# Performance work log

Hardware: AMD Instinct MI355X
Metric: run time of the kernel (lower is better)

## Reference

```python
import jax, jax.numpy as jnp
import numpy as np

EPS = 1e-6
NEG = -1e9
W = 8          # chunk_size
H_MA = 4       # monotonic heads
H_CA = 1       # chunkwise heads
ADIM = 1024
SHARP = 1.0    # sharpening_factor
SCALE = float(np.sqrt(ADIM))


def moving_sum(x, back, forward):
    # windowed sum over last axis, window = back+forward+1 (small, fixed)
    K = x.shape[-1]
    pad = [(0, 0)] * (x.ndim - 1) + [(back, forward)]
    xp = jnp.pad(x, pad)
    out = xp[..., 0:K]
    for d in range(1, back + forward + 1):
        out = out + xp[..., d:d + K]
    return out


def exclusive_cumsum(x):
    z = jnp.zeros(x.shape[:-1] + (1,), x.dtype)
    return jnp.cumsum(jnp.concatenate([z, x[..., :-1]], axis=-1), axis=-1)


def setup_inputs():
    key0 = jax.random.key(0)
    ks = jax.random.split(key0, 12)
    B, K, Q, D = 16, 2000, 256, 1024
    nrm = lambda k, shp, s=1.0: jax.random.normal(k, shp, jnp.float32) * s
    aw_prev = jnp.zeros((B, H_MA, 1, K), jnp.float32).at[..., 0].set(1.0)
    return {
        'key': nrm(ks[0], (B, K, D)),
        'value': nrm(ks[1], (B, K, D)),
        'query': nrm(ks[2], (B, Q, D)),
        'mask': jnp.ones((B, Q, K), jnp.int32),
        'aw_prev': aw_prev,
        'Wk_ma': nrm(ks[3], (D, ADIM), 0.02), 'bk_ma': jnp.zeros((ADIM,), jnp.float32),
        'Wq_ma': nrm(ks[4], (D, ADIM), 0.02), 'bq_ma': jnp.zeros((ADIM,), jnp.float32),
        'r': jnp.full((1,), -4.0, jnp.float32),
        'Wk_ca': nrm(ks[5], (D, ADIM), 0.02), 'bk_ca': jnp.zeros((ADIM,), jnp.float32),
        'Wq_ca': nrm(ks[6], (D, ADIM), 0.02), 'bq_ca': jnp.zeros((ADIM,), jnp.float32),
        'Wv': nrm(ks[7], (D, ADIM), 0.02), 'bv': jnp.zeros((ADIM,), jnp.float32),
        'Wo': nrm(ks[8], (ADIM, D), 0.02), 'bo': jnp.zeros((D,), jnp.float32),
    }


def reference(key, value, query, mask, aw_prev,
              Wk_ma, bk_ma, Wq_ma, bq_ma, r,
              Wk_ca, bk_ca, Wq_ca, bq_ca, Wv, bv, Wo, bo):
    B, K, D = key.shape
    Q = query.shape[1]
    dk_ma = ADIM // H_MA
    H_tot = H_MA * H_CA
    dk_ca = ADIM // H_tot
    m = (mask[:, None] != 0)  # [B,1,Q,K]

    # ---- monotonic energy: [B,H_ma,Q,K]
    k_ma = (key @ Wk_ma + bk_ma).reshape(B, K, H_MA, dk_ma)
    q_ma = (query @ Wq_ma + bq_ma).reshape(B, Q, H_MA, dk_ma)
    e_ma = jnp.einsum('bqhd,bkhd->bhqk', q_ma, k_ma) / SCALE + r[0]
    e_ma = jnp.where(m, e_ma, NEG)

    # ---- monotonic alignment alpha (parallel training mode)
    p = jax.nn.sigmoid(e_ma)                                  # [B,H,Q,K]
    log1mp = jnp.log(jnp.clip(1.0 - p, EPS, 1.0))
    cp = jnp.exp(exclusive_cumsum(log1mp))                    # safe_cumprod(1-p)

    def step(aw, pc):
        p_i, cp_i = pc                                        # [B,H,K]
        denom = jnp.clip(cp_i, EPS, 1.0)
        aw_new = p_i * cp_i * jnp.cumsum(aw / denom, axis=-1)
        return aw_new, aw_new

    xs = (p.transpose(2, 0, 1, 3), cp.transpose(2, 0, 1, 3))  # [Q,B,H,K]
    _, alphas = jax.lax.scan(step, aw_prev[:, :, 0], xs)
    alpha = alphas.transpose(1, 2, 0, 3)                      # [B,H_ma,Q,K]

    # ---- chunk energy: [B,H_ma*H_ca,Q,K]
    k_ca = (key @ Wk_ca + bk_ca).reshape(B, K, H_tot, dk_ca)
    q_ca = (query @ Wq_ca + bq_ca).reshape(B, Q, H_tot, dk_ca)
    e_ca = jnp.einsum('bqhd,bkhd->bhqk', q_ca, k_ca) / SCALE
    e_ca = jnp.where(m, e_ca, NEG)

    # ---- soft chunkwise attention (moving-sum windowed softmax)
    u = e_ca.reshape(B, H_MA, H_CA, Q, K)
    a5 = alpha[:, :, None] * SHARP                            # [B,H_ma,1,Q,K]
    u = u - jnp.max(u, axis=-1, keepdims=True)
    se = jnp.clip(jnp.exp(u), 1e-5, None)
    denom = moving_sum(se, W - 1, 0)
    beta = se * moving_sum(a5 / denom, 0, W - 1)
    beta = beta.reshape(B, H_tot, Q, K)

    # ---- context + output projection
    v = (value @ Wv + bv).reshape(B, K, H_tot, dk_ca)
    cv = jnp.einsum('bhqk,bkhd->bqhd', beta, v).reshape(B, Q, ADIM)
    return cv @ Wo + bo
```

## Files before the change

### kernel.cpp

```cpp
#include <hip/hip_runtime.h>


typedef __bf16 bf16x8_t __attribute__((ext_vector_type(8)));
typedef float f32x4_t __attribute__((ext_vector_type(4)));
typedef unsigned short ushort8_t __attribute__((ext_vector_type(8)));
typedef unsigned short ushort4_t __attribute__((ext_vector_type(4)));
typedef unsigned int uint4_t __attribute__((ext_vector_type(4)));

__device__ __forceinline__ unsigned short f2bf(float x) {
  unsigned int u = __builtin_bit_cast(unsigned int, x);
  u += 0x7fffu + ((u >> 16) & 1u);
  return (unsigned short)(u >> 16);
}
__device__ __forceinline__ float bf2f(unsigned short h) {
  unsigned int u = ((unsigned int)h) << 16;
  return __builtin_bit_cast(float, u);
}

__device__ __forceinline__ void gld16(const unsigned short* g, unsigned short* l) {
  __builtin_amdgcn_global_load_lds(
      (const __attribute__((address_space(1))) void*)g,
      (__attribute__((address_space(3))) void*)l, 16, 0, 0);
}

__device__ __forceinline__ float wave_incl_scan(float x) {
  float v = x;
  int mv;
#define DPP_ADD(ctrl, rmask, bctrl)                                           \
  mv = __builtin_amdgcn_update_dpp(0, __builtin_bit_cast(int, v), ctrl,       \
                                   rmask, 0xf, bctrl);                        \
  v += __builtin_bit_cast(float, mv);
  DPP_ADD(0x111, 0xf, true);
  DPP_ADD(0x112, 0xf, true);
  DPP_ADD(0x114, 0xf, true);
  DPP_ADD(0x118, 0xf, true);
  DPP_ADD(0x142, 0xa, false);
  DPP_ADD(0x143, 0xc, false);
#undef DPP_ADD
  return v;
}

__device__ __forceinline__ float wave_max_bcast(float x) {
  const float NI = -__builtin_inff();
  float v = x;
  int mv;
#define DPP_MAX(ctrl, rmask)                                                  \
  mv = __builtin_amdgcn_update_dpp(__builtin_bit_cast(int, NI),               \
                                   __builtin_bit_cast(int, v), ctrl, rmask,   \
                                   0xf, false);                               \
  v = fmaxf(v, __builtin_bit_cast(float, mv));
  DPP_MAX(0x111, 0xf) DPP_MAX(0x112, 0xf) DPP_MAX(0x114, 0xf)
  DPP_MAX(0x118, 0xf) DPP_MAX(0x142, 0xa) DPP_MAX(0x143, 0xc)
#undef DPP_MAX
  int r = __builtin_amdgcn_readlane(__builtin_bit_cast(int, v), 63);
  return __builtin_bit_cast(float, r);
}

#define WSHR1(dst, src)                                                       \
  {                                                                           \
    int _t = __builtin_amdgcn_update_dpp(0, __builtin_bit_cast(int, src),     \
                                         0x138, 0xf, 0xf, true);              \
    dst = __builtin_bit_cast(float, _t);                                      \
  }
#define WSHL1(dst, src)                                                       \
  {                                                                           \
    int _t = __builtin_amdgcn_update_dpp(0, __builtin_bit_cast(int, src),     \
                                         0x130, 0xf, 0xf, true);              \
    dst = __builtin_bit_cast(float, _t);                                      \
  }

__device__ __forceinline__ void gemm_bt_tile(
    const unsigned short* __restrict__ A, long lda,
    const unsigned short* __restrict__ B, long ldb,
    int Kd, unsigned short* lA, unsigned short* lB, f32x4_t acc[4][4]) {
  const int tid = threadIdx.x;
  const int lane = tid & 63;
  const int wid = tid >> 6;
  const int wm = wid >> 1, wn = wid & 1;
  const int lr = lane & 15, quad = lane >> 4;
  const int srow = wid * 32 + (lane >> 3);
  const int scol = ((lane & 7) ^ (lane >> 3)) * 8;
  const int rs = lr & 7;
  for (int ks = 0; ks < Kd; ks += 64) {
    __syncthreads();
    const unsigned short* Ag = A + (long)srow * lda + ks + scol;
    const unsigned short* Bg = B + (long)srow * ldb + ks + scol;
#pragma unroll
    for (int r = 0; r < 4; ++r) {
      gld16(Ag + (long)(r * 8) * lda, lA + (wid * 32 + r * 8) * 64);
      gld16(Bg + (long)(r * 8) * ldb, lB + (wid * 32 + r * 8) * 64);
    }
    __syncthreads();
#pragma unroll
    for (int kk = 0; kk < 2; ++kk) {
      bf16x8_t afr[4], bfr[4];
#pragma unroll
      for (int i = 0; i < 4; ++i)
        afr[i] = *(const bf16x8_t*)(lA + (wm * 64 + i * 16 + lr) * 64 +
                                    (((kk * 4 + quad) ^ rs) << 3));
#pragma unroll
      for (int j = 0; j < 4; ++j)
        bfr[j] = *(const bf16x8_t*)(lB + (wn * 64 + j * 16 + lr) * 64 +
                                    (((kk * 4 + quad) ^ rs) << 3));
#pragma unroll
      for (int i = 0; i < 4; ++i)
#pragma unroll
        for (int j = 0; j < 4; ++j)
          acc[i][j] = __builtin_amdgcn_mfma_f32_16x16x32_bf16(afr[i], bfr[j], acc[i][j], 0, 0, 0);
    }
  }
}

#define EPILOGUE_IDX()                                          \
  const int tid = threadIdx.x, lane = tid & 63, wid = tid >> 6; \
  const int wm = wid >> 1, wn = wid & 1, lr = lane & 15, quad = lane >> 4;

#define ACC_INIT()                              \
  f32x4_t acc[4][4];                            \
  _Pragma("unroll") for (int i = 0; i < 4; ++i) \
  _Pragma("unroll") for (int j = 0; j < 4; ++j) \
  _Pragma("unroll") for (int r = 0; r < 4; ++r) acc[i][j][r] = 0.f;

__device__ __forceinline__ void epi_stash(float* lT, f32x4_t (&acc)[4][4],
                                          int i, int wm, int wn, int lr, int quad) {
#pragma unroll
  for (int j = 0; j < 4; ++j) {
    int lcol = wn * 64 + j * 16 + lr;
#pragma unroll
    for (int r = 0; r < 4; ++r) {
      int lrow = wm * 16 + quad * 4 + r;
      lT[lrow * 128 + (((lcol >> 2) ^ (lrow & 7)) << 2) + (lcol & 3)] = acc[i][j][r];
    }
  }
}
__device__ __forceinline__ f32x4_t epi_read(const float* lT, int rloc, int col4) {
  return *(const f32x4_t*)&lT[rloc * 128 + ((col4 ^ (rloc & 7)) << 2)];
}

__global__ __launch_bounds__(256) void k_proj(const unsigned short* __restrict__ A,
                                              const unsigned short* __restrict__ Wt,
                                              const float* __restrict__ bias,
                                              unsigned short* __restrict__ C) {
  __shared__ __attribute__((aligned(16))) char smem[32768];
  unsigned short* lA = (unsigned short*)smem;
  unsigned short* lB = (unsigned short*)(smem + 16384);
  float* lT = (float*)smem;
  ACC_INIT();
  int flat = blockIdx.x;
  int mb = (flat >> 6) * 8 + (flat & 7);
  int nb = (flat >> 3) & 7;
  const unsigned short* Ab = A + (long)mb * 128 * 1024;
  const unsigned short* Bb = Wt + (long)nb * 128 * 1024;
  gemm_bt_tile(Ab, 1024, Bb, 1024, 1024, lA, lB, acc);
  EPILOGUE_IDX();
  (void)lane;
  long mbase = (long)mb * 128;
  int nbase = nb * 128;
  const int rloc = tid >> 3, c7 = tid & 7;
#pragma unroll
  for (int i = 0; i < 4; ++i) {
    __syncthreads();
    epi_stash(lT, acc, i, wm, wn, lr, quad);
    __syncthreads();
    long mg = mbase + (rloc >> 4) * 64 + i * 16 + (rloc & 15);
    unsigned short* crow = C + mg * 1024 + nbase;
    const float* brow = bias + nbase;
#pragma unroll
    for (int m = 0; m < 4; ++m) {
      int col4 = c7 + 8 * m;
      f32x4_t v = epi_read(lT, rloc, col4);
      f32x4_t bv = *(const f32x4_t*)&brow[col4 * 4];
      ushort4_t o;
#pragma unroll
      for (int z = 0; z < 4; ++z) o[z] = f2bf(v[z] + bv[z]);
      *(ushort4_t*)(crow + col4 * 4) = o;
    }
  }
}

__global__ __launch_bounds__(256) void k_maskpack(const int* __restrict__ mask,
                                                  unsigned int* __restrict__ mw) {
  int lane = threadIdx.x & 63, wid = threadIdx.x >> 6;
  int row = blockIdx.x * 4 + wid;
  const int* mp = mask + (long)row * 2000;
  unsigned int* op = mw + (long)row * 64;
  for (int c = 0; c < 32; ++c) {
    int k = c * 64 + lane;
    int v = (k < 2000) ? mp[k] : 0;
    unsigned long long b = __ballot(v != 0);
    if (lane == 0) {
      op[c * 2] = (unsigned int)b;
      op[c * 2 + 1] = (unsigned int)(b >> 32);
    }
  }
}

__global__ __launch_bounds__(256) void k_escore(const unsigned short* __restrict__ qproj,
                                                const unsigned short* __restrict__ kproj,
                                                const unsigned int* __restrict__ maskw,
                                                const float* __restrict__ rptr,
                                                unsigned short* __restrict__ outp, int is_ma) {
  __shared__ __attribute__((aligned(16))) char smem[32768];
  unsigned short* lA = (unsigned short*)smem;
  unsigned short* lB = (unsigned short*)(smem + 16384);
  float* lT = (float*)smem;
  ACC_INIT();
  int bz = blockIdx.z, b = bz >> 2, h = bz & 3;
  int nrow0 = blockIdx.x * 128;
  const unsigned short* Ab = qproj + ((long)b * 256 + blockIdx.y * 128) * 1024 + h * 256;
  const unsigned short* Bb = kproj + ((long)b * 2048 + nrow0) * 1024 + h * 256;
  gemm_bt_tile(Ab, 1024, Bb, 1024, 256, lA, lB, acc);
  float rv = is_ma ? rptr[0] : 0.f;
  EPILOGUE_IDX();
  (void)lane;
  const int rloc = tid >> 3, c7 = tid & 7;
#pragma unroll
  for (int i = 0; i < 4; ++i) {
    __syncthreads();
    epi_stash(lT, acc, i, wm, wn, lr, quad);
    __syncthreads();
    int qg = blockIdx.y * 128 + (rloc >> 4) * 64 + i * 16 + (rloc & 15);
    uint4_t mw4 = *(const uint4_t*)(maskw + (((long)b * 256 + qg) << 6) + (nrow0 >> 5));
    unsigned short* orow = outp + ((long)bz * 256 + qg) * 2048 + nrow0;
#pragma unroll
    for (int m = 0; m < 4; ++m) {
      int col4 = c7 + 8 * m;
      f32x4_t v = epi_read(lT, rloc, col4);
      unsigned int bits = (mw4[m] >> (4 * c7)) & 0xFu;
      ushort4_t o;
#pragma unroll
      for (int z = 0; z < 4; ++z) {
        float e = v[z] * 0.03125f;
        bool valid = (bits >> z) & 1u;
        float ov;
        if (is_ma)
          ov = valid ? (1.f / (1.f + __expf(-(e + rv)))) : 0.f;
        else
          ov = valid ? e : -1e9f;
        o[z] = f2bf(ov);
      }
      *(ushort4_t*)(orow + col4 * 4) = o;
    }
  }
}

__global__ __launch_bounds__(256) void k_cp(const unsigned short* __restrict__ p,
                                            unsigned short* __restrict__ cp) {
  __shared__ float wsum[4];
  long base = (long)blockIdx.x * 2048;
  int tid = threadIdx.x, lane = tid & 63, wid = tid >> 6;
  ushort8_t p8 = *(const ushort8_t*)(p + base + tid * 8);
  float lex[8], s1 = 0.f;
#pragma unroll
  for (int i = 0; i < 8; ++i) {
    float om = fminf(fmaxf(1.f - bf2f((unsigned short)p8[i]), 1e-6f), 1.f);
    lex[i] = s1;
    s1 += __logf(om);
  }
  float incl = wave_incl_scan(s1);
  if (lane == 63) wsum[wid] = incl;
  __syncthreads();
  float off = incl - s1;
  if (wid > 0) off += wsum[0];
  if (wid > 1) off += wsum[1];
  if (wid > 2) off += wsum[2];
  ushort8_t o;
#pragma unroll
  for (int i = 0; i < 8; ++i) o[i] = f2bf(__expf(off + lex[i]));
  *(ushort8_t*)(cp + base + tid * 8) = o;
}

__global__ __launch_bounds__(256) void k_scan(const unsigned short* __restrict__ p,
                                              const unsigned short* cp,
                                              const float* __restrict__ awp,
                                              unsigned short* alpha) {
  __shared__ float wsum[2][4];
  int bh = blockIdx.x;
  int tid = threadIdx.x, lane = tid & 63, wid = tid >> 6;
  long base = (long)bh * 256 * 2048 + tid * 8;
  float aw[8];
  const float* ap = awp + (long)bh * 2000;
#pragma unroll
  for (int i = 0; i < 8; ++i) {
    int k = tid * 8 + i;
    aw[i] = (k < 2000) ? ap[k] : 0.f;
  }
  const unsigned short* prow = p + base;
  const unsigned short* crow = cp + base;
  unsigned short* arow = alpha + base;
  ushort8_t pbuf[4], cbuf[4];
#pragma unroll
  for (int s = 0; s < 4; ++s) {
    pbuf[s] = *(const ushort8_t*)(prow + (long)s * 2048);
    cbuf[s] = *(const ushort8_t*)(crow + (long)s * 2048);
  }
  for (int qo = 0; qo < 256; qo += 4) {
#pragma unroll
    for (int s = 0; s < 4; ++s) {
      const int q = qo + s;
      ushort8_t pcur = pbuf[s], ccur = cbuf[s];
      if (q + 4 < 256) {
        pbuf[s] = *(const ushort8_t*)(prow + (long)(q + 4) * 2048);
        cbuf[s] = *(const ushort8_t*)(crow + (long)(q + 4) * 2048);
      }
      float pc[8], rd[8];
#pragma unroll
      for (int i = 0; i < 8; ++i) {
        float pv = bf2f((unsigned short)pcur[i]);
        float cv = bf2f((unsigned short)ccur[i]);
        pc[i] = pv * cv;
        rd[i] = __builtin_amdgcn_rcpf(fminf(fmaxf(cv, 1e-6f), 1.f));
      }
      float t[8], s1 = 0.f;
#pragma unroll
      for (int i = 0; i < 8; ++i) {
        s1 = fmaf(aw[i], rd[i], s1);
        t[i] = s1;
      }
      float incl = wave_incl_scan(s1);
      if (lane == 63) wsum[q & 1][wid] = incl;
      __syncthreads();
      float off = incl - s1;
      if (wid > 0) off += wsum[q & 1][0];
      if (wid > 1) off += wsum[q & 1][1];
      if (wid > 2) off += wsum[q & 1][2];
      ushort8_t o;
#pragma unroll
      for (int i = 0; i < 8; ++i) {
        aw[i] = pc[i] * (t[i] + off);
        o[i] = f2bf(aw[i]);
      }
      *(ushort8_t*)(arow + (long)q * 2048) = o;
    }
  }
}

__global__ __launch_bounds__(256) void k_beta(unsigned short* eca,
                                              const unsigned short* __restrict__ alpha) {
  __shared__ float red[4];
  __shared__ float edgeB[4][8];
  __shared__ float edgeF[4][8];
  long base = (long)blockIdx.x * 2048 + threadIdx.x * 8;
  int tid = threadIdx.x, lane = tid & 63, wid = tid >> 6;
  (void)tid;
  ushort8_t u8 = *(const ushort8_t*)(eca + base);
  ushort8_t a8 = *(const ushort8_t*)(alpha + base);
  float u[8], a[8];
#pragma unroll
  for (int i = 0; i < 8; ++i) {
    u[i] = bf2f((unsigned short)u8[i]);
    a[i] = bf2f((unsigned short)a8[i]);
  }
  float m = u[0];
#pragma unroll
  for (int i = 1; i < 8; ++i) m = fmaxf(m, u[i]);
  m = wave_max_bcast(m);
  if (lane == 0) red[wid] = m;
  __syncthreads();
  m = fmaxf(fmaxf(red[0], red[1]), fmaxf(red[2], red[3]));
  float se[8], lp[8];
  float s = 0.f;
#pragma unroll
  for (int i = 0; i < 8; ++i) {
    se[i] = fmaxf(__expf(u[i] - m), 1e-5f);
    s += se[i];
    lp[i] = s;
  }
  float plp[8];
#pragma unroll
  for (int i = 0; i < 8; ++i) WSHR1(plp[i], lp[i]);
  if (lane == 63) {
#pragma unroll
    for (int i = 0; i < 8; ++i) edgeB[wid][i] = lp[i];
  }
  __syncthreads();
  if (lane == 0 && wid > 0) {
#pragma unroll
    for (int i = 0; i < 8; ++i) plp[i] = edgeB[wid - 1][i];
  }
  float sra[8], lf[8];
  s = 0.f;
#pragma unroll
  for (int i = 0; i < 8; ++i) {
    float msb = lp[i] + plp[7] - plp[i];
    sra[i] = a[i] * __builtin_amdgcn_rcpf(msb);
    s += sra[i];
    lf[i] = s;
  }
  float nlf[8];
#pragma unroll
  for (int i = 0; i < 8; ++i) WSHL1(nlf[i], lf[i]);
  if (lane == 0) {
#pragma unroll
    for (int i = 0; i < 8; ++i) edgeF[wid][i] = lf[i];
  }
  __syncthreads();
  if (lane == 63 && wid < 3) {
#pragma unroll
    for (int i = 0; i < 8; ++i) nlf[i] = edgeF[wid + 1][i];
  }
  ushort8_t o;
#pragma unroll
  for (int i = 0; i < 8; ++i) {
    float own = lf[7] - (i ? lf[i - 1] : 0.f);
    float nxt = i ? nlf[i - 1] : 0.f;
    o[i] = f2bf(se[i] * (own + nxt));
  }
  *(ushort8_t*)(eca + base) = o;
}

__global__ __launch_bounds__(256) void k_build_vT(const unsigned short* __restrict__ v,
                                                  unsigned short* __restrict__ vT) {
  __shared__ unsigned short t[64][68];
  int bz = blockIdx.z, b = bz >> 2, h = bz & 3;
  int k0 = blockIdx.x * 64, d0 = blockIdx.y * 64;
  int tx = threadIdx.x & 63, tg = threadIdx.x >> 6;
#pragma unroll
  for (int i = 0; i < 16; ++i) {
    int kk = tg * 16 + i;
    t[kk][tx] = v[((long)(b * 2048 + k0 + kk)) * 1024 + h * 256 + d0 + tx];
  }
  __syncthreads();
#pragma unroll
  for (int i = 0; i < 16; ++i) {
    int dd = tg * 16 + i;
    vT[((long)bz * 256 + d0 + dd) * 2048 + k0 + tx] = t[tx][dd];
  }
}

__global__ __launch_bounds__(256) void k_cv(const unsigned short* __restrict__ beta,
                                            const unsigned short* __restrict__ vT,
                                            unsigned short* __restrict__ cv) {
  __shared__ __attribute__((aligned(16))) char smem[32768];
  unsigned short* lA = (unsigned short*)smem;
  unsigned short* lB = (unsigned short*)(smem + 16384);
  float* lT = (float*)smem;
  ACC_INIT();
  int bz = blockIdx.z, b = bz >> 2, h = bz & 3;
  const unsigned short* Ab = beta + (long)bz * 256 * 2048 + (long)blockIdx.y * 128 * 2048;
  const unsigned short* Bb = vT + (long)bz * 256 * 2048 + (long)blockIdx.x * 128 * 2048;
  gemm_bt_tile(Ab, 2048, Bb, 2048, 2048, lA, lB, acc);
  EPILOGUE_IDX();
  (void)lane;
  const int rloc = tid >> 3, c7 = tid & 7;
#pragma unroll
  for (int i = 0; i < 4; ++i) {
    __syncthreads();
    epi_stash(lT, acc, i, wm, wn, lr, quad);
    __syncthreads();
    long mg = (long)b * 256 + blockIdx.y * 128 + (rloc >> 4) * 64 + i * 16 + (rloc & 15);
    unsigned short* crow = cv + mg * 1024 + h * 256 + blockIdx.x * 128;
#pragma unroll
    for (int m = 0; m < 4; ++m) {
      int col4 = c7 + 8 * m;
      f32x4_t v = epi_read(lT, rloc, col4);
      ushort4_t o;
#pragma unroll
      for (int z = 0; z < 4; ++z) o[z] = f2bf(v[z]);
      *(ushort4_t*)(crow + col4 * 4) = o;
    }
  }
}

__global__ __launch_bounds__(256) void k_out(const unsigned short* __restrict__ cv,
                                             const unsigned short* __restrict__ WoT,
                                             const float* __restrict__ bo,
                                             float* __restrict__ outp) {
  __shared__ __attribute__((aligned(16))) char smem[32768];
  unsigned short* lA = (unsigned short*)smem;
  unsigned short* lB = (unsigned short*)(smem + 16384);
  float* lT = (float*)smem;
  ACC_INIT();
  const unsigned short* Ab = cv + (long)blockIdx.y * 128 * 1024;
  const unsigned short* Bb = WoT + (long)blockIdx.x * 128 * 1024;
  gemm_bt_tile(Ab, 1024, Bb, 1024, 1024, lA, lB, acc);
  EPILOGUE_IDX();
  (void)lane;
  const int rloc = tid >> 3, c7 = tid & 7;
#pragma unroll
  for (int i = 0; i < 4; ++i) {
    __syncthreads();
    epi_stash(lT, acc, i, wm, wn, lr, quad);
    __syncthreads();
    long mg = (long)blockIdx.y * 128 + (rloc >> 4) * 64 + i * 16 + (rloc & 15);
    float* orow = outp + mg * 1024 + blockIdx.x * 128;
    const float* brow = bo + blockIdx.x * 128;
#pragma unroll
    for (int m = 0; m < 4; ++m) {
      int col4 = c7 + 8 * m;
      f32x4_t v = epi_read(lT, rloc, col4);
      f32x4_t bv = *(const f32x4_t*)&brow[col4 * 4];
      *(f32x4_t*)&orow[col4 * 4] = v + bv;
    }
  }
}

__global__ __launch_bounds__(256) void k_twT(const float* __restrict__ W,
                                             unsigned short* __restrict__ Wt) {
  __shared__ float t[32][33];
  int bx = blockIdx.x, by = blockIdx.y;
  int lx = threadIdx.x & 31, ly = threadIdx.x >> 5;
#pragma unroll
  for (int r = 0; r < 4; ++r)
    t[ly + 8 * r][lx] = W[((long)(by * 32 + ly + 8 * r)) * 1024 + bx * 32 + lx];
  __syncthreads();
#pragma unroll
  for (int r = 0; r < 4; ++r)
    Wt[((long)(bx * 32 + ly + 8 * r)) * 1024 + by * 32 + lx] = f2bf(t[lx][ly + 8 * r]);
}

__global__ __launch_bounds__(256) void k_cvt_pad(const float* __restrict__ src,
                                                 unsigned short* __restrict__ dst) {
  long idx = (long)blockIdx.x * 256 + threadIdx.x;
  int b = (int)(idx >> 18);
  int rem = (int)(idx & 262143);
  int row = rem >> 7;
  int c8 = rem & 127;
  ushort8_t o;
  if (row < 2000) {
    const float* sp = src + ((long)(b * 2000 + row)) * 1024 + c8 * 8;
    float4 f0 = *(const float4*)sp;
    float4 f1 = *(const float4*)(sp + 4);
    o[0] = f2bf(f0.x); o[1] = f2bf(f0.y); o[2] = f2bf(f0.z); o[3] = f2bf(f0.w);
    o[4] = f2bf(f1.x); o[5] = f2bf(f1.y); o[6] = f2bf(f1.z); o[7] = f2bf(f1.w);
  } else {
#pragma unroll
    for (int z = 0; z < 8; ++z) o[z] = 0;
  }
  *(ushort8_t*)(dst + idx * 8) = o;
}

__global__ __launch_bounds__(256) void k_cvt(const float* __restrict__ src,
                                             unsigned short* __restrict__ dst) {
  long idx = (long)blockIdx.x * 256 + threadIdx.x;
  const float* sp = src + idx * 8;
  float4 f0 = *(const float4*)sp;
  float4 f1 = *(const float4*)(sp + 4);
  ushort8_t o;
  o[0] = f2bf(f0.x); o[1] = f2bf(f0.y); o[2] = f2bf(f0.z); o[3] = f2bf(f0.w);
  o[4] = f2bf(f1.x); o[5] = f2bf(f1.y); o[6] = f2bf(f1.z); o[7] = f2bf(f1.w);
  *(ushort8_t*)(dst + idx * 8) = o;
}

extern "C" void kernel_launch(void* const* d_in, const int* in_sizes, int n_in,
                              void* d_out, int out_size, void* d_ws, size_t ws_size,
                              hipStream_t stream) {
  const float* key = (const float*)d_in[0];
  const float* value = (const float*)d_in[1];
  const float* query = (const float*)d_in[2];
  const int* mask = (const int*)d_in[3];
  const float* awp = (const float*)d_in[4];
  const float* Wk_ma = (const float*)d_in[5];
  const float* bk_ma = (const float*)d_in[6];
  const float* Wq_ma = (const float*)d_in[7];
  const float* bq_ma = (const float*)d_in[8];
  const float* rvec = (const float*)d_in[9];
  const float* Wk_ca = (const float*)d_in[10];
  const float* bk_ca = (const float*)d_in[11];
  const float* Wq_ca = (const float*)d_in[12];
  const float* bq_ca = (const float*)d_in[13];
  const float* Wv = (const float*)d_in[14];
  const float* bv = (const float*)d_in[15];
  const float* Wo = (const float*)d_in[16];
  const float* bo = (const float*)d_in[17];
  float* outp = (float*)d_out;
  (void)in_sizes; (void)n_in; (void)out_size;

  char* ws = (char*)d_ws;
  size_t off = 0;
  auto alloc = [&](size_t bytes) {
    void* pp = ws + off;
    off += (bytes + 255) & ~(size_t)255;
    return pp;
  };
  unsigned short* wt[6];
  for (int i = 0; i < 6; ++i) wt[i] = (unsigned short*)alloc(1024L * 1024 * 2);
  unsigned short* xbf = (unsigned short*)alloc(16L * 2048 * 1024 * 2);
  unsigned short* qbf = (unsigned short*)alloc(4096L * 1024 * 2);
  unsigned short* kproj = (unsigned short*)alloc(16L * 2048 * 1024 * 2);
  unsigned short* qproj = (unsigned short*)alloc(4096L * 1024 * 2);
  unsigned short* bufP = (unsigned short*)alloc(64L * 256 * 2048 * 2);
  unsigned short* bufA = (unsigned short*)alloc(64L * 256 * 2048 * 2);
  unsigned int* maskw = (unsigned int*)alloc(4096L * 64 * 4);
  if (ws_size < off) return;
  unsigned short* cv_bf = qbf;

  dim3 blk(256);
  k_twT<<<dim3(32, 32), blk, 0, stream>>>(Wk_ma, wt[0]);
  k_twT<<<dim3(32, 32), blk, 0, stream>>>(Wq_ma, wt[1]);
  k_twT<<<dim3(32, 32), blk, 0, stream>>>(Wk_ca, wt[2]);
  k_twT<<<dim3(32, 32), blk, 0, stream>>>(Wq_ca, wt[3]);
  k_twT<<<dim3(32, 32), blk, 0, stream>>>(Wv, wt[4]);
  k_twT<<<dim3(32, 32), blk, 0, stream>>>(Wo, wt[5]);
  k_maskpack<<<dim3(1024), blk, 0, stream>>>(mask, maskw);
  k_cvt_pad<<<dim3(16384), blk, 0, stream>>>(key, xbf);
  k_cvt<<<dim3(2048), blk, 0, stream>>>(query, qbf);
  k_proj<<<dim3(2048), blk, 0, stream>>>(xbf, wt[0], bk_ma, kproj);
  k_proj<<<dim3(256), blk, 0, stream>>>(qbf, wt[1], bq_ma, qproj);
  k_escore<<<dim3(16, 2, 64), blk, 0, stream>>>(qproj, kproj, maskw, rvec, bufP, 1);
  k_cp<<<dim3(16384), blk, 0, stream>>>(bufP, bufA);
  k_proj<<<dim3(2048), blk, 0, stream>>>(xbf, wt[2], bk_ca, kproj);
  k_proj<<<dim3(256), blk, 0, stream>>>(qbf, wt[3], bq_ca, qproj);
  k_scan<<<dim3(64), blk, 0, stream>>>(bufP, bufA, awp, bufA);
  k_escore<<<dim3(16, 2, 64), blk, 0, stream>>>(qproj, kproj, maskw, rvec, bufP, 0);
  k_beta<<<dim3(16384), blk, 0, stream>>>(bufP, bufA);
  k_cvt_pad<<<dim3(16384), blk, 0, stream>>>(value, xbf);
  k_proj<<<dim3(2048), blk, 0, stream>>>(xbf, wt[4], bv, kproj);
  k_build_vT<<<dim3(32, 4, 64), blk, 0, stream>>>(kproj, bufA);
  k_cv<<<dim3(2, 2, 64), blk, 0, stream>>>(bufP, bufA, cv_bf);
  k_out<<<dim3(8, 32), blk, 0, stream>>>(cv_bf, wt[5], bo, outp);
}
```

Before: 1.033 ms.

## Stage scan inputs through double-buffered LDS with async global-to-LDS loads

The sequential monotonic scan kernel now prefetches p and cumprod rows two at a time into double-buffered shared memory using global_load_lds, instead of holding four rows in registers. Each of the four waves loads a quarter of one row pair. The per-row barrier is replaced by an explicit lgkmcnt wait plus s_barrier, which avoids a full vmcnt wait on every step. The aim is to hide global latency on the serial q loop without register pressure, at the cost of extra barriers and tricky vmcnt accounting, since outstanding stores count toward the vmcnt(2) wait.

```diff
diff --git a/kernel.cpp b/kernel.cpp
--- a/kernel.cpp
+++ b/kernel.cpp
@@ -274,10 +274,12 @@
                                               const unsigned short* cp,
                                               const float* __restrict__ awp,
                                               unsigned short* alpha) {
+  __shared__ unsigned short lsp[2][2][2048];
+  __shared__ unsigned short lsc[2][2][2048];
   __shared__ float wsum[2][4];
   int bh = blockIdx.x;
-  int tid = threadIdx.x, lane = tid & 63, wid = tid >> 6;
-  long base = (long)bh * 256 * 2048 + tid * 8;
+  int tid = threadIdx.x, lane = tid & 63, w = tid >> 6;
+  long base = (long)bh * 256 * 2048;
   float aw[8];
   const float* ap = awp + (long)bh * 2000;
 #pragma unroll
@@ -285,29 +287,36 @@
     int k = tid * 8 + i;
     aw[i] = (k < 2000) ? ap[k] : 0.f;
   }
-  const unsigned short* prow = p + base;
-  const unsigned short* crow = cp + base;
-  unsigned short* arow = alpha + base;
-  ushort8_t pbuf[4], cbuf[4];
-#pragma unroll
-  for (int s = 0; s < 4; ++s) {
-    pbuf[s] = *(const ushort8_t*)(prow + (long)s * 2048);
-    cbuf[s] = *(const ushort8_t*)(crow + (long)s * 2048);
-  }
-  for (int qo = 0; qo < 256; qo += 4) {
-#pragma unroll
-    for (int s = 0; s < 4; ++s) {
-      const int q = qo + s;
-      ushort8_t pcur = pbuf[s], ccur = cbuf[s];
-      if (q + 4 < 256) {
-        pbuf[s] = *(const ushort8_t*)(prow + (long)(q + 4) * 2048);
-        cbuf[s] = *(const ushort8_t*)(crow + (long)(q + 4) * 2048);
-      }
+  const unsigned short* pg = p + base;
+  const unsigned short* cg = cp + base;
+  unsigned short* ag = alpha + base;
+  const int sa = w >> 1;
+  const int sr = w & 1;
+  const unsigned short* sbase = (sa ? cg : pg) + (long)sr * 2048 + lane * 8;
+#define STAGE(c, b)                                                           \
+  {                                                                           \
+    const unsigned short* _src = sbase + (long)(c) * 2 * 2048;                \
+    unsigned short* _dst = sa ? &lsc[b][sr][0] : &lsp[b][sr][0];              \
+    _Pragma("unroll") for (int _q = 0; _q < 4; ++_q)                          \
+        gld16(_src + _q * 512, _dst + _q * 512);                              \
+  }
+  STAGE(0, 0);
+  asm volatile("s_waitcnt vmcnt(0)" ::: "memory");
+  __builtin_amdgcn_s_barrier();
+  asm volatile("" ::: "memory");
+  for (int c = 0; c < 128; ++c) {
+    const int b = c & 1;
+    if (c < 127) STAGE(c + 1, b ^ 1);
+#pragma unroll
+    for (int cr = 0; cr < 2; ++cr) {
+      const int q = c * 2 + cr;
+      ushort8_t p8 = *(const ushort8_t*)&lsp[b][cr][tid * 8];
+      ushort8_t c8 = *(const ushort8_t*)&lsc[b][cr][tid * 8];
       float pc[8], rd[8];
 #pragma unroll
       for (int i = 0; i < 8; ++i) {
-        float pv = bf2f((unsigned short)pcur[i]);
-        float cv = bf2f((unsigned short)ccur[i]);
+        float pv = bf2f((unsigned short)p8[i]);
+        float cv = bf2f((unsigned short)c8[i]);
         pc[i] = pv * cv;
         rd[i] = __builtin_amdgcn_rcpf(fminf(fmaxf(cv, 1e-6f), 1.f));
       }
@@ -318,21 +327,27 @@
         t[i] = s1;
       }
       float incl = wave_incl_scan(s1);
-      if (lane == 63) wsum[q & 1][wid] = incl;
-      __syncthreads();
+      if (lane == 63) wsum[q & 1][w] = incl;
+      asm volatile("s_waitcnt lgkmcnt(0)" ::: "memory");
+      __builtin_amdgcn_s_barrier();
+      asm volatile("" ::: "memory");
       float off = incl - s1;
-      if (wid > 0) off += wsum[q & 1][0];
-      if (wid > 1) off += wsum[q & 1][1];
-      if (wid > 2) off += wsum[q & 1][2];
+      if (w > 0) off += wsum[q & 1][0];
+      if (w > 1) off += wsum[q & 1][1];
+      if (w > 2) off += wsum[q & 1][2];
       ushort8_t o;
 #pragma unroll
       for (int i = 0; i < 8; ++i) {
         aw[i] = pc[i] * (t[i] + off);
         o[i] = f2bf(aw[i]);
       }
-      *(ushort8_t*)(arow + (long)q * 2048) = o;
-    }
-  }
+      *(ushort8_t*)(ag + (long)q * 2048 + tid * 8) = o;
+    }
+    asm volatile("s_waitcnt vmcnt(2)" ::: "memory");
+    __builtin_amdgcn_s_barrier();
+    asm volatile("" ::: "memory");
+  }
+#undef STAGE
 }
 
 __global__ __launch_bounds__(256) void k_beta(unsigned short* eca,
```

Result: no change. 1.031 ms (-0.2%).
